# Performance work log

Hardware: AMD Instinct MI355X
Metric: run time of the kernel (lower is better)

## Reference

```python
import jax, jax.numpy as jnp
import numpy as np

K = 12          # tagset size incl START/STOP
START = 10
STOP = 11
NEG = -10000.0
B, T, V, D, H = 64, 1024, 50000, 256, 512
Hh = H // 2


def setup_inputs() -> dict:
    key = jax.random.key(0)
    ks = jax.random.split(key, 20)
    sentence = jax.random.randint(ks[0], (B, T), 1, V)
    seq_lens = jax.random.randint(ks[1], (B,), T // 2, T + 1)
    emb = jax.random.normal(ks[2], (V, D), dtype=jnp.float32) * 0.1
    emb = emb.at[0].set(0.0)  # padding_idx=0
    s = 1.0 / np.sqrt(Hh)

    def u(k, shape):
        return jax.random.uniform(k, shape, minval=-s, maxval=s, dtype=jnp.float32)

    Wih_f = u(ks[3], (4 * Hh, D)); Whh_f = u(ks[4], (4 * Hh, Hh))
    bih_f = u(ks[5], (4 * Hh,));  bhh_f = u(ks[6], (4 * Hh,))
    Wih_b = u(ks[7], (4 * Hh, D)); Whh_b = u(ks[8], (4 * Hh, Hh))
    bih_b = u(ks[9], (4 * Hh,));  bhh_b = u(ks[10], (4 * Hh,))
    sl = 1.0 / np.sqrt(H)
    Wtag = jax.random.uniform(ks[11], (K, H), minval=-sl, maxval=sl, dtype=jnp.float32)
    btag = jax.random.uniform(ks[12], (K,), minval=-sl, maxval=sl, dtype=jnp.float32)
    transitions = jax.random.normal(ks[13], (K, K), dtype=jnp.float32)
    transitions = transitions.at[START, :].set(NEG).at[:, STOP].set(NEG)
    h0 = jax.random.normal(ks[14], (2, B, Hh), dtype=jnp.float32)
    c0 = jax.random.normal(ks[15], (2, B, Hh), dtype=jnp.float32)
    return dict(sentence=sentence, seq_lens=seq_lens, emb=emb,
                Wih_f=Wih_f, Whh_f=Whh_f, bih_f=bih_f, bhh_f=bhh_f,
                Wih_b=Wih_b, Whh_b=Whh_b, bih_b=bih_b, bhh_b=bhh_b,
                Wtag=Wtag, btag=btag, transitions=transitions, h0=h0, c0=c0)


def _lstm_dir(x, mask, h0, c0, Wih, Whh, bih, bhh, reverse):
    # x: [B,T,D], mask: [B,T] bool. Masked steps keep the carried state
    # (equivalent to PyTorch packed-sequence semantics for positions < seq_len).
    def step(carry, inp):
        h, c = carry
        xt, mt = inp  # [B,D], [B,1]
        z = xt @ Wih.T + h @ Whh.T + bih + bhh  # [B,4Hh], torch gate order i,f,g,o
        i, f, g, o = jnp.split(z, 4, axis=-1)
        c2 = jax.nn.sigmoid(f) * c + jax.nn.sigmoid(i) * jnp.tanh(g)
        h2 = jax.nn.sigmoid(o) * jnp.tanh(c2)
        h = jnp.where(mt, h2, h)
        c = jnp.where(mt, c2, c)
        return (h, c), h
    xs = (x.transpose(1, 0, 2), mask.T[:, :, None])
    _, hs = jax.lax.scan(step, (h0, c0), xs, reverse=reverse)
    return hs.transpose(1, 0, 2)  # [B,T,Hh]


def reference(sentence, seq_lens, emb, Wih_f, Whh_f, bih_f, bhh_f,
              Wih_b, Whh_b, bih_b, bhh_b, Wtag, btag, transitions, h0, c0):
    Bn, Tn = sentence.shape
    mask = jnp.arange(Tn)[None, :] < seq_lens[:, None]  # [B,T]
    x = emb[sentence]  # [B,T,D]
    hf = _lstm_dir(x, mask, h0[0], c0[0], Wih_f, Whh_f, bih_f, bhh_f, False)
    hb = _lstm_dir(x, mask, h0[1], c0[1], Wih_b, Whh_b, bih_b, bhh_b, True)
    feats = jnp.concatenate([hf, hb], -1) @ Wtag.T + btag  # [B,T,K]

    # Vectorized Viterbi over batch and tags (replaces per-tag python loops)
    fv0 = jnp.full((Bn, K), NEG, dtype=feats.dtype).at[:, START].set(0.0)
    ident = jnp.arange(K)[None, :]

    def vstep(fv, inp):
        ft, mt = inp  # [B,K], [B]
        sc = fv[:, None, :] + transitions[None, :, :]  # [B,Knext,Kprev]
        bp = jnp.argmax(sc, -1)                        # [B,K]
        vmax = jnp.max(sc, -1) + ft
        fv2 = jnp.where(mt[:, None], vmax, fv)
        bp = jnp.where(mt[:, None], bp, ident)         # identity passthrough on pad
        return fv2, bp

    fv, bptrs = jax.lax.scan(vstep, fv0, (feats.transpose(1, 0, 2), mask.T))
    term = fv + transitions[STOP][None, :]
    best = jnp.argmax(term, -1)   # [B]
    score = jnp.max(term, -1)     # [B]

    def btrace(tag, bp):
        prev = jnp.take_along_axis(bp, tag[:, None], 1)[:, 0]
        return prev, tag

    _, path = jax.lax.scan(btrace, best, bptrs, reverse=True)  # [T,B]
    path = jnp.where(mask, path.T, 0)  # [B,T], zeros beyond seq_len
    return score, path
```

## Files before the change

### kernel.cpp

```cpp
#include <hip/hip_runtime.h>
#include <math.h>

#define NEG10K -10000.0f

static const size_t OFF_WT_IH = 0;
static const size_t OFF_WT_HH = 524288;
static const size_t OFF_BIAS  = 1048576;
static const size_t OFF_WTAGD = 1050624;
static const size_t OFF_BTAG  = 1058816;
static const size_t OFF_FEATS = 1058832;
static const size_t OFF_HC    = 3155984;
static const size_t OFF_CC    = 3188752;
static const size_t OFF_PUB   = 3221520;
static const size_t OFF_END   = 3352592;

__device__ __forceinline__ float sigf(float x) { return 1.0f / (1.0f + expf(-x)); }

__global__ __launch_bounds__(256) void k_transpose(
    const float* __restrict__ wih_f, const float* __restrict__ wih_b,
    const float* __restrict__ whh_f, const float* __restrict__ whh_b,
    float* __restrict__ ws) {
  __shared__ float tile[32][33];
  int z = blockIdx.z;
  const float* src = (z == 0) ? wih_f : (z == 1) ? wih_b : (z == 2) ? whh_f : whh_b;
  float* dst = ws + ((z < 2) ? (OFF_WT_IH + (size_t)z * 262144)
                             : (OFF_WT_HH + (size_t)(z - 2) * 262144));
  int r0 = blockIdx.y * 32;
  int c0 = blockIdx.x * 32;
  int tid = threadIdx.x;
  int c = tid & 31, rg = tid >> 5;
#pragma unroll
  for (int i = 0; i < 4; ++i) {
    int r = rg * 4 + i;
    tile[r][c] = src[(size_t)(r0 + r) * 256 + c0 + c];
  }
  __syncthreads();
  int r2 = tid & 31, cg = tid >> 5;
#pragma unroll
  for (int i = 0; i < 4; ++i) {
    int ccv = cg * 4 + i;
    dst[(size_t)(c0 + ccv) * 1024 + r0 + r2] = tile[r2][ccv];
  }
}

__global__ __launch_bounds__(256) void k_prep_small(
    const float* __restrict__ bih_f, const float* __restrict__ bhh_f,
    const float* __restrict__ bih_b, const float* __restrict__ bhh_b,
    const float* __restrict__ wtag, const float* __restrict__ btag,
    float* __restrict__ ws) {
  int i = blockIdx.x * 256 + threadIdx.x;
  if (i < 2048) {
    int d = i >> 10, n = i & 1023;
    ws[OFF_BIAS + i] = d ? (bih_b[n] + bhh_b[n]) : (bih_f[n] + bhh_f[n]);
  } else if (i < 2048 + 8192) {
    int r = i - 2048;
    int d = r >> 12, rem = r & 4095;
    int k = rem >> 8, j = rem & 255;
    ws[OFF_WTAGD + r] = (k < 12) ? wtag[(size_t)k * 512 + d * 256 + j] : 0.0f;
  } else if (i < 2048 + 8192 + 16) {
    int kk = i - 10240;
    ws[OFF_BTAG + kk] = (kk < 12) ? btag[kk] : 0.0f;
  } else if (i < 10256 + 131072) {
    ws[OFF_PUB + (i - 10256)] = 0.0f;
  }
}

#define FMA4(A, W, S) { A.x = fmaf(W.x, S, A.x); A.y = fmaf(W.y, S, A.y); \
                        A.z = fmaf(W.z, S, A.z); A.w = fmaf(W.w, S, A.w); }
__global__ __launch_bounds__(512, 2) void k_lstm_split(
    const float* __restrict__ ws_c, const int* __restrict__ sentence,
    const float* __restrict__ emb, const float* __restrict__ h0p,
    const float* __restrict__ c0p, const int* __restrict__ seq_lens,
    float* __restrict__ ws_mut, int first) {
  __shared__ float zpart[8][4][128];
  __shared__ float zs[4][128];
  __shared__ float h_s[4][256];
  __shared__ float x_s[2][4][256];
  __shared__ int   sent_s[4][1024];
  __shared__ float ldspad[10240];

  int bx = blockIdx.x;
  int w   = (bx >> 3) & 7;
  int gid = (bx & 7) + ((bx >> 6) << 3);
  int d   = gid >> 4;
  int bq4 = (gid & 15) * 4;
  int u0  = w * 32;
  int tid = threadIdx.x;
  if (first == 777) {
    ldspad[tid] = (float)tid; __syncthreads(); zs[0][0] = ldspad[tid ^ 1];
  }

  int cg = tid & 31, kq = tid >> 5;
  int c4 = cg * 4;
  int wv = tid >> 6, ln = tid & 63;

  for (int i = tid; i < 4096; i += 512)
    sent_s[i >> 10][i & 1023] = sentence[(size_t)(bq4 + (i >> 10)) * 1024 + (i & 1023)];
  __syncthreads();

  const float* WhhT = ws_c + OFF_WT_HH + (size_t)d * 262144;
  const float* WihT = ws_c + OFF_WT_IH + (size_t)d * 262144;
  int wcol = (cg >> 3) * 256 + u0 + (cg & 7) * 4;
  float4 wh[16], wi[16];
#pragma unroll
  for (int i = 0; i < 16; ++i) {
    wh[i] = *(const float4*)(WhhT + (size_t)(kq * 16 + i) * 1024 + wcol);
    wi[i] = *(const float4*)(WihT + (size_t)(kq * 16 + i) * 1024 + wcol);
  }

  for (int i = tid; i < 1024; i += 512) {
    int b = i >> 8, u = i & 255;
    h_s[b][u] = h0p[((size_t)d * 64 + bq4 + b) * 256 + u];
  }
  float cc = 0.0f; int mylen = 0;
  int ob = tid >> 5, ou = tid & 31;
  if (tid < 128) {
    cc = c0p[((size_t)d * 64 + bq4 + ob) * 256 + u0 + ou];
    mylen = seq_lens[bq4 + ob];
  }
  int bB = tid >> 7, jB = tid & 127;
  int colB = ((jB >> 5) << 8) + u0 + (jB & 31);
  float biasB = ws_c[OFF_BIAS + (size_t)d * 1024 + colB];
  int xb = tid >> 7, xj = (tid & 127) * 2;
  {
    int tt = d ? 1023 : 0;
    float2 v = *(const float2*)(emb + (size_t)sent_s[xb][tt] * 256 + xj);
    x_s[0][xb][xj] = v.x; x_s[0][xb][xj + 1] = v.y;
  }
  int tb_b = wv >> 1;
  int tb_k = (wv & 1) * 8 + (ln >> 3);
  int tb_j = ln & 7;
  float wtag_r[32];
  {
    const float* wtg = ws_c + OFF_WTAGD + (size_t)d * 4096 + tb_k * 256;
#pragma unroll
    for (int i = 0; i < 32; ++i) wtag_r[i] = wtg[tb_j + 8 * i];
  }
  unsigned long long* pub64 = (unsigned long long*)(ws_mut + OFF_PUB);
  float* featsD = ws_mut + OFF_FEATS + (size_t)d * 1048576;
  int gb = tid >> 8, gu = tid & 255;
  bool bail = false;
  __syncthreads();

  float4 acc_carry[4] = {{0,0,0,0},{0,0,0,0},{0,0,0,0},{0,0,0,0}};
#pragma unroll
  for (int i = 0; i < 4; ++i) {
    int k = kq * 16 + i * 4;
    float4 q0 = wi[i * 4], q1 = wi[i * 4 + 1], q2 = wi[i * 4 + 2], q3 = wi[i * 4 + 3];
#pragma unroll
    for (int b = 0; b < 4; ++b) {
      float4 xv = *(const float4*)&x_s[0][b][k];
      FMA4(acc_carry[b], q0, xv.x); FMA4(acc_carry[b], q1, xv.y);
      FMA4(acc_carry[b], q2, xv.z); FMA4(acc_carry[b], q3, xv.w);
    }
  }

  for (int s = 0; s < 1024; ++s) {
    int t = d ? (1023 - s) : s;
    int p = s & 1;
    int cur = s & 1, nxt = cur ^ 1;
    unsigned tag = (unsigned)(s + 1);
    float2 xpf;
    {
      int sn = (s + 1 < 1024) ? (s + 1) : s;
      int tn = d ? (1023 - sn) : sn;
      xpf = *(const float2*)(emb + (size_t)sent_s[xb][tn] * 256 + xj);
    }
    float4 acc[4];
#pragma unroll
    for (int b = 0; b < 4; ++b) acc[b] = acc_carry[b];
#pragma unroll
    for (int i = 0; i < 4; ++i) {
      int k = kq * 16 + i * 4;
      float4 w0 = wh[i * 4], w1 = wh[i * 4 + 1], w2 = wh[i * 4 + 2], w3 = wh[i * 4 + 3];
#pragma unroll
      for (int b = 0; b < 4; ++b) {
        float4 hv = *(const float4*)&h_s[b][k];
        FMA4(acc[b], w0, hv.x); FMA4(acc[b], w1, hv.y);
        FMA4(acc[b], w2, hv.z); FMA4(acc[b], w3, hv.w);
      }
    }
#pragma unroll
    for (int b = 0; b < 4; ++b) {
      acc[b].x += __shfl_xor(acc[b].x, 32);
      acc[b].y += __shfl_xor(acc[b].y, 32);
      acc[b].z += __shfl_xor(acc[b].z, 32);
      acc[b].w += __shfl_xor(acc[b].w, 32);
    }
    if ((tid & 32) == 0) {
#pragma unroll
      for (int b = 0; b < 4; ++b) *(float4*)&zpart[wv][b][c4] = acc[b];
    }
    __syncthreads();
    zs[bB][jB] = zpart[0][bB][jB] + zpart[1][bB][jB] + zpart[2][bB][jB] + zpart[3][bB][jB] +
                 zpart[4][bB][jB] + zpart[5][bB][jB] + zpart[6][bB][jB] + zpart[7][bB][jB] + biasB;
    x_s[nxt][xb][xj] = xpf.x; x_s[nxt][xb][xj + 1] = xpf.y;
    __syncthreads();
    if (tid < 128) {
      float zi = zs[ob][ou], zf = zs[ob][32 + ou], zg = zs[ob][64 + ou], zo = zs[ob][96 + ou];
      float cn = sigf(zf) * cc + sigf(zi) * tanhf(zg);
      float hn = sigf(zo) * tanhf(cn);
      bool m = t < mylen;
      cc = m ? cn : cc;
      float hp = m ? hn : h_s[ob][u0 + ou];
      union { float f; unsigned u; } hb; hb.f = hp;
      unsigned long long pk = ((unsigned long long)tag << 32) | (unsigned long long)hb.u;
      __hip_atomic_store(
          pub64 + (size_t)p * 32768 + ((size_t)d * 64 + bq4 + ob) * 256 + (u0 + ou),
          pk, __ATOMIC_RELAXED, __HIP_MEMORY_SCOPE_AGENT);
    }
    if (s > 0) {
      int tp = d ? (1023 - (s - 1)) : (s - 1);
      float pv = 0.0f;
#pragma unroll
      for (int i = 0; i < 32; ++i)
        pv = fmaf(h_s[tb_b][tb_j + 8 * i], wtag_r[i], pv);
      pv += __shfl_xor(pv, 1);
      pv += __shfl_xor(pv, 2);
      pv += __shfl_xor(pv, 4);
      if (w == 0 && tb_j == 0)
        featsD[(size_t)(bq4 + tb_b) * 16384 + (size_t)tp * 16 + tb_k] = pv;
    }
    __syncthreads();
    {
      size_t base = (size_t)p * 32768 + ((size_t)d * 64 + bq4) * 256;
      size_t i0 = base + (size_t)gb * 256 + gu;
      size_t i1 = i0 + 512;
      unsigned long long v0 =
          __hip_atomic_load(pub64 + i0, __ATOMIC_RELAXED, __HIP_MEMORY_SCOPE_AGENT);
      unsigned long long v1 =
          __hip_atomic_load(pub64 + i1, __ATOMIC_RELAXED, __HIP_MEMORY_SCOPE_AGENT);
      if (s + 1 < 1024) {
#pragma unroll
        for (int b = 0; b < 4; ++b) { acc_carry[b].x = 0; acc_carry[b].y = 0;
                                      acc_carry[b].z = 0; acc_carry[b].w = 0; }
#pragma unroll
        for (int i = 0; i < 4; ++i) {
          int k = kq * 16 + i * 4;
          float4 q0 = wi[i * 4], q1 = wi[i * 4 + 1], q2 = wi[i * 4 + 2], q3 = wi[i * 4 + 3];
#pragma unroll
          for (int b = 0; b < 4; ++b) {
            float4 xv = *(const float4*)&x_s[nxt][b][k];
            FMA4(acc_carry[b], q0, xv.x); FMA4(acc_carry[b], q1, xv.y);
            FMA4(acc_carry[b], q2, xv.z); FMA4(acc_carry[b], q3, xv.w);
          }
        }
      }
      unsigned spin = 0;
      while ((((unsigned)(v0 >> 32) != tag) || ((unsigned)(v1 >> 32) != tag)) && !bail) {
        __builtin_amdgcn_s_sleep(1);
        if ((unsigned)(v0 >> 32) != tag)
          v0 = __hip_atomic_load(pub64 + i0, __ATOMIC_RELAXED, __HIP_MEMORY_SCOPE_AGENT);
        if ((unsigned)(v1 >> 32) != tag)
          v1 = __hip_atomic_load(pub64 + i1, __ATOMIC_RELAXED, __HIP_MEMORY_SCOPE_AGENT);
        if (++spin > 2000000u) { bail = true; break; }
      }
      union { unsigned u32; float f; } cv0, cv1;
      cv0.u32 = (unsigned)v0; cv1.u32 = (unsigned)v1;
      h_s[gb][gu]     = cv0.f;
      h_s[gb + 2][gu] = cv1.f;
    }
    __syncthreads();
  }
  {
    float pv = 0.0f;
#pragma unroll
    for (int i = 0; i < 32; ++i)
      pv = fmaf(h_s[tb_b][tb_j + 8 * i], wtag_r[i], pv);
    pv += __shfl_xor(pv, 1);
    pv += __shfl_xor(pv, 2);
    pv += __shfl_xor(pv, 4);
    int tl = d ? 0 : 1023;
    if (w == 0 && tb_j == 0)
      featsD[(size_t)(bq4 + tb_b) * 16384 + (size_t)tl * 16 + tb_k] = pv;
  }
}

__global__ __launch_bounds__(256) void k_lstm_fused(
    const float* __restrict__ ws_c, const int* __restrict__ sentence,
    const float* __restrict__ emb, const float* __restrict__ h0p,
    const float* __restrict__ c0p, const int* __restrict__ seq_lens,
    float* __restrict__ ws_mut) {
  int d = blockIdx.x & 1;
  int pr = blockIdx.x >> 1;
  int b0 = pr * 2, b1 = b0 + 1;
  const float* Wih = ws_c + OFF_WT_IH + (size_t)d * 262144;
  const float* Whh = ws_c + OFF_WT_HH + (size_t)d * 262144;
  __shared__ float h_s[2][256];
  __shared__ float x_s[2][2][256];
  __shared__ float z_s[2][1024];
  __shared__ int   sent_s[2][1024];
  __shared__ float wt_s[16][260];
  __shared__ float pfp_s[2][16][8];
  int tid = threadIdx.x;
  int len0 = seq_lens[b0], len1 = seq_lens[b1];
  for (int i = tid; i < 2048; i += 256)
    sent_s[i >> 10][i & 1023] = sentence[(size_t)(b0 + (i >> 10)) * 1024 + (i & 1023)];
  for (int i = tid; i < 4096; i += 256)
    wt_s[i >> 8][i & 255] = ws_c[OFF_WTAGD + (size_t)d * 4096 + i];
  h_s[0][tid] = h0p[((size_t)d * 64 + b0) * 256 + tid];
  h_s[1][tid] = h0p[((size_t)d * 64 + b1) * 256 + tid];
  float cc0 = c0p[((size_t)d * 64 + b0) * 256 + tid];
  float cc1 = c0p[((size_t)d * 64 + b1) * 256 + tid];
  int c4 = tid * 4;
  float4 bias_v = *(const float4*)(ws_c + OFF_BIAS + (size_t)d * 1024 + c4);
  __syncthreads();
  int t0 = d ? 1023 : 0;
  if (tid < 128) {
    int bb = tid >> 6, l = tid & 63;
    int row = sent_s[bb][t0];
    *(float4*)&x_s[0][bb][l * 4] = *(const float4*)(emb + (size_t)row * 256 + l * 4);
  }
  __syncthreads();
  float* featsD = ws_mut + OFF_FEATS + (size_t)d * 1048576;
  for (int s = 0; s < 1024; ++s) {
    int t = d ? (1023 - s) : s;
    int cur = s & 1, nxt = cur ^ 1;
    float4 pf = {0, 0, 0, 0};
    if (tid < 128) {
      int sn = (s < 1023) ? (s + 1) : 1023;
      int tn = d ? (1023 - sn) : sn;
      int bb = tid >> 6, l = tid & 63;
      pf = *(const float4*)(emb + (size_t)sent_s[bb][tn] * 256 + l * 4);
    }
    float4 a0 = bias_v, a1 = bias_v;
#pragma unroll 4
    for (int k = 0; k < 256; k += 4) {
      float4 xv0 = *(const float4*)&x_s[cur][0][k];
      float4 xv1 = *(const float4*)&x_s[cur][1][k];
      float4 hv0 = *(const float4*)&h_s[0][k];
      float4 hv1 = *(const float4*)&h_s[1][k];
      const float* wi = Wih + (size_t)k * 1024 + c4;
      const float* wh = Whh + (size_t)k * 1024 + c4;
      float4 wi0 = *(const float4*)(wi);
      float4 wi1 = *(const float4*)(wi + 1024);
      float4 wi2 = *(const float4*)(wi + 2048);
      float4 wi3 = *(const float4*)(wi + 3072);
      float4 wh0 = *(const float4*)(wh);
      float4 wh1 = *(const float4*)(wh + 1024);
      float4 wh2 = *(const float4*)(wh + 2048);
      float4 wh3 = *(const float4*)(wh + 3072);
      FMA4(a0, wi0, xv0.x); FMA4(a0, wi1, xv0.y); FMA4(a0, wi2, xv0.z); FMA4(a0, wi3, xv0.w);
      FMA4(a0, wh0, hv0.x); FMA4(a0, wh1, hv0.y); FMA4(a0, wh2, hv0.z); FMA4(a0, wh3, hv0.w);
      FMA4(a1, wi0, xv1.x); FMA4(a1, wi1, xv1.y); FMA4(a1, wi2, xv1.z); FMA4(a1, wi3, xv1.w);
      FMA4(a1, wh0, hv1.x); FMA4(a1, wh1, hv1.y); FMA4(a1, wh2, hv1.z); FMA4(a1, wh3, hv1.w);
    }
    *(float4*)&z_s[0][c4] = a0;
    *(float4*)&z_s[1][c4] = a1;
    __syncthreads();
    {
      float iv = z_s[0][tid], fv = z_s[0][tid + 256];
      float gv = z_s[0][tid + 512], ov = z_s[0][tid + 768];
      float cn = sigf(fv) * cc0 + sigf(iv) * tanhf(gv);
      float hn = sigf(ov) * tanhf(cn);
      bool m = t < len0;
      cc0 = m ? cn : cc0;
      h_s[0][tid] = m ? hn : h_s[0][tid];
    }
    {
      float iv = z_s[1][tid], fv = z_s[1][tid + 256];
      float gv = z_s[1][tid + 512], ov = z_s[1][tid + 768];
      float cn = sigf(fv) * cc1 + sigf(iv) * tanhf(gv);
      float hn = sigf(ov) * tanhf(cn);
      bool m = t < len1;
      cc1 = m ? cn : cc1;
      h_s[1][tid] = m ? hn : h_s[1][tid];
    }
    if (tid < 128) {
      int bb = tid >> 6, l = tid & 63;
      *(float4*)&x_s[nxt][bb][l * 4] = pf;
    }
    __syncthreads();
    {
      int b2 = tid >> 7, r = tid & 127;
      int ks = r >> 3, jg = r & 7;
      const float* hv = &h_s[b2][jg * 32];
      const float* wv = &wt_s[ks][jg * 32];
      float p = 0.0f;
#pragma unroll
      for (int i = 0; i < 32; ++i) p = fmaf(hv[i], wv[i], p);
      pfp_s[b2][ks][jg] = p;
    }
    __syncthreads();
    if (tid < 32) {
      int b = tid >> 4, k = tid & 15;
      float sum = 0.0f;
#pragma unroll
      for (int i = 0; i < 8; ++i) sum += pfp_s[b][k][i];
      featsD[(size_t)(b0 + b) * 16384 + (size_t)t * 16 + k] = sum;
    }
  }
}

__global__ __launch_bounds__(64) void k_viterbi(const float* __restrict__ ws_c,
                                                const float* __restrict__ trans,
                                                const int* __restrict__ seq_lens,
                                                float* __restrict__ out) {
  __shared__ char bp_s[1024][12];
  int b = blockIdx.x, lane = threadIdx.x;
  int len = seq_lens[b];
  float trow[12];
#pragma unroll
  for (int p = 0; p < 12; ++p) trow[p] = (lane < 12) ? trans[lane * 12 + p] : 0.0f;
  float tb = (lane < 16) ? ws_c[OFF_BTAG + lane] : 0.0f;
  float fv = (lane == 10) ? 0.0f : NEG10K;
  const float* ff = ws_c + OFF_FEATS + (size_t)b * 16384;
  const float* fb = ws_c + OFF_FEATS + 1048576 + (size_t)b * 16384;
  for (int t = 0; t < 1024; ++t) {
    float ft = (lane < 16) ? (ff[t * 16 + lane] + fb[t * 16 + lane] + tb) : 0.0f;
    float best = -3.0e38f; int arg = 0;
#pragma unroll
    for (int p = 0; p < 12; ++p) {
      float s = __shfl(fv, p) + trow[p];
      if (s > best) { best = s; arg = p; }
    }
    bool m = t < len;
    if (m) fv = best + ft;
    if (lane < 12) bp_s[t][lane] = (char)(m ? arg : lane);
  }
  float term = (lane < 12) ? fv + trans[132 + lane] : -3.0e38f;
  float bestv = -3.0e38f; int bestp = 0;
#pragma unroll
  for (int p = 0; p < 12; ++p) {
    float v = __shfl(term, p);
    if (v > bestv) { bestv = v; bestp = p; }
  }
  __syncthreads();
  if (lane == 0) {
    out[b] = bestv;
    int tag = bestp;
    float* po = out + 64 + (size_t)b * 1024;
    for (int t = 1023; t >= 0; --t) {
      po[t] = (t < len) ? (float)tag : 0.0f;
      tag = bp_s[t][tag];
    }
  }
}

extern "C" void kernel_launch(void* const* d_in, const int* in_sizes, int n_in,
                              void* d_out, int out_size, void* d_ws, size_t ws_size,
                              hipStream_t stream) {
  (void)in_sizes; (void)n_in; (void)out_size;
  const int*   sentence = (const int*)d_in[0];
  const int*   seq_lens = (const int*)d_in[1];
  const float* emb      = (const float*)d_in[2];
  const float* wih_f    = (const float*)d_in[3];
  const float* whh_f    = (const float*)d_in[4];
  const float* bih_f    = (const float*)d_in[5];
  const float* bhh_f    = (const float*)d_in[6];
  const float* wih_b    = (const float*)d_in[7];
  const float* whh_b    = (const float*)d_in[8];
  const float* bih_b    = (const float*)d_in[9];
  const float* bhh_b    = (const float*)d_in[10];
  const float* wtag     = (const float*)d_in[11];
  const float* btag     = (const float*)d_in[12];
  const float* trans    = (const float*)d_in[13];
  const float* h0p      = (const float*)d_in[14];
  const float* c0p      = (const float*)d_in[15];
  float* ws  = (float*)d_ws;
  float* out = (float*)d_out;
  size_t avail = ws_size / 4;
  if (avail < OFF_FEATS + 2097152) return;

  k_transpose<<<dim3(8, 32, 4), 256, 0, stream>>>(wih_f, wih_b, whh_f, whh_b, ws);
  k_prep_small<<<553, 256, 0, stream>>>(bih_f, bhh_f, bih_b, bhh_b, wtag, btag, ws);
  if (avail >= OFF_END) {
    k_lstm_split<<<256, 512, 0, stream>>>(ws, sentence, emb, h0p, c0p, seq_lens, ws, 1);
  } else {
    k_lstm_fused<<<64, 256, 0, stream>>>(ws, sentence, emb, h0p, c0p, seq_lens, ws);
  }
  k_viterbi<<<64, 64, 0, stream>>>(ws, trans, seq_lens, out);
}
```

Baseline: 3.650 ms.

## Split LSTM recurrence across 512 blocks of 256 threads with 16 units each

Re-partitions the persistent split LSTM kernel so each block owns 16 hidden units instead of 32. The grid doubles to 512 blocks of 256 threads, halving per-block work per timestep and the per-step reduction depth. The tag projection weights move from registers into shared memory and only w==0 blocks compute feats. The cost is twice as many blocks taking part in the cross-block spin-wait exchange every step, and each thread now polls four published values instead of two.

```diff
diff --git a/kernel.cpp b/kernel.cpp
--- a/kernel.cpp
+++ b/kernel.cpp
@@ -67,40 +67,44 @@
 
 #define FMA4(A, W, S) { A.x = fmaf(W.x, S, A.x); A.y = fmaf(W.y, S, A.y); \
                         A.z = fmaf(W.z, S, A.z); A.w = fmaf(W.w, S, A.w); }
-__global__ __launch_bounds__(512, 2) void k_lstm_split(
+__global__ __launch_bounds__(256, 2) void k_lstm_split(
     const float* __restrict__ ws_c, const int* __restrict__ sentence,
     const float* __restrict__ emb, const float* __restrict__ h0p,
     const float* __restrict__ c0p, const int* __restrict__ seq_lens,
     float* __restrict__ ws_mut, int first) {
-  __shared__ float zpart[8][4][128];
-  __shared__ float zs[4][128];
+  __shared__ float zpart[4][4][64];
+  __shared__ float zs[4][64];
   __shared__ float h_s[4][256];
   __shared__ float x_s[2][4][256];
   __shared__ int   sent_s[4][1024];
-  __shared__ float ldspad[10240];
+  __shared__ float wt_s[16][260];
+  __shared__ float ldspad[6400];
 
   int bx = blockIdx.x;
-  int w   = (bx >> 3) & 7;
-  int gid = (bx & 7) + ((bx >> 6) << 3);
+  int w   = (bx >> 3) & 15;
+  int gid = (bx & 7) + ((bx >> 7) << 3);
   int d   = gid >> 4;
   int bq4 = (gid & 15) * 4;
-  int u0  = w * 32;
+  int u0  = w * 16;
   int tid = threadIdx.x;
+  int ln  = tid & 63;
   if (first == 777) {
     ldspad[tid] = (float)tid; __syncthreads(); zs[0][0] = ldspad[tid ^ 1];
   }
 
-  int cg = tid & 31, kq = tid >> 5;
+  int cg = tid & 15, kq = tid >> 4;
   int c4 = cg * 4;
-  int wv = tid >> 6, ln = tid & 63;
-
-  for (int i = tid; i < 4096; i += 512)
+  int wv = tid >> 6;
+
+  for (int i = tid; i < 4096; i += 256)
     sent_s[i >> 10][i & 1023] = sentence[(size_t)(bq4 + (i >> 10)) * 1024 + (i & 1023)];
+  for (int i = tid; i < 4096; i += 256)
+    wt_s[i >> 8][i & 255] = ws_c[OFF_WTAGD + (size_t)d * 4096 + i];
   __syncthreads();
 
   const float* WhhT = ws_c + OFF_WT_HH + (size_t)d * 262144;
   const float* WihT = ws_c + OFF_WT_IH + (size_t)d * 262144;
-  int wcol = (cg >> 3) * 256 + u0 + (cg & 7) * 4;
+  int wcol = (cg >> 2) * 256 + u0 + (cg & 3) * 4;
   float4 wh[16], wi[16];
 #pragma unroll
   for (int i = 0; i < 16; ++i) {
@@ -108,37 +112,23 @@
     wi[i] = *(const float4*)(WihT + (size_t)(kq * 16 + i) * 1024 + wcol);
   }
 
-  for (int i = tid; i < 1024; i += 512) {
-    int b = i >> 8, u = i & 255;
-    h_s[b][u] = h0p[((size_t)d * 64 + bq4 + b) * 256 + u];
-  }
+  for (int i = tid; i < 1024; i += 256)
+    h_s[i >> 8][i & 255] = h0p[((size_t)d * 64 + bq4 + (i >> 8)) * 256 + (i & 255)];
   float cc = 0.0f; int mylen = 0;
-  int ob = tid >> 5, ou = tid & 31;
-  if (tid < 128) {
+  int ob = tid >> 4, ou = tid & 15;
+  if (tid < 64) {
     cc = c0p[((size_t)d * 64 + bq4 + ob) * 256 + u0 + ou];
     mylen = seq_lens[bq4 + ob];
   }
-  int bB = tid >> 7, jB = tid & 127;
-  int colB = ((jB >> 5) << 8) + u0 + (jB & 31);
-  float biasB = ws_c[OFF_BIAS + (size_t)d * 1024 + colB];
-  int xb = tid >> 7, xj = (tid & 127) * 2;
+  int bB = tid >> 6, jB = tid & 63;
+  float biasB = ws_c[OFF_BIAS + (size_t)d * 1024 + (jB >> 4) * 256 + u0 + (jB & 15)];
+  int xb = tid >> 6, xj = (tid & 63) * 4;
   {
     int tt = d ? 1023 : 0;
-    float2 v = *(const float2*)(emb + (size_t)sent_s[xb][tt] * 256 + xj);
-    x_s[0][xb][xj] = v.x; x_s[0][xb][xj + 1] = v.y;
-  }
-  int tb_b = wv >> 1;
-  int tb_k = (wv & 1) * 8 + (ln >> 3);
-  int tb_j = ln & 7;
-  float wtag_r[32];
-  {
-    const float* wtg = ws_c + OFF_WTAGD + (size_t)d * 4096 + tb_k * 256;
-#pragma unroll
-    for (int i = 0; i < 32; ++i) wtag_r[i] = wtg[tb_j + 8 * i];
+    *(float4*)&x_s[0][xb][xj] = *(const float4*)(emb + (size_t)sent_s[xb][tt] * 256 + xj);
   }
   unsigned long long* pub64 = (unsigned long long*)(ws_mut + OFF_PUB);
   float* featsD = ws_mut + OFF_FEATS + (size_t)d * 1048576;
-  int gb = tid >> 8, gu = tid & 255;
   bool bail = false;
   __syncthreads();
 
@@ -158,13 +148,13 @@
   for (int s = 0; s < 1024; ++s) {
     int t = d ? (1023 - s) : s;
     int p = s & 1;
-    int cur = s & 1, nxt = cur ^ 1;
+    int nxt = (s & 1) ^ 1;
     unsigned tag = (unsigned)(s + 1);
-    float2 xpf;
+    float4 xpf;
     {
       int sn = (s + 1 < 1024) ? (s + 1) : s;
       int tn = d ? (1023 - sn) : sn;
-      xpf = *(const float2*)(emb + (size_t)sent_s[xb][tn] * 256 + xj);
+      xpf = *(const float4*)(emb + (size_t)sent_s[xb][tn] * 256 + xj);
     }
     float4 acc[4];
 #pragma unroll
@@ -182,22 +172,26 @@
     }
 #pragma unroll
     for (int b = 0; b < 4; ++b) {
+      acc[b].x += __shfl_xor(acc[b].x, 16);
+      acc[b].y += __shfl_xor(acc[b].y, 16);
+      acc[b].z += __shfl_xor(acc[b].z, 16);
+      acc[b].w += __shfl_xor(acc[b].w, 16);
       acc[b].x += __shfl_xor(acc[b].x, 32);
       acc[b].y += __shfl_xor(acc[b].y, 32);
       acc[b].z += __shfl_xor(acc[b].z, 32);
       acc[b].w += __shfl_xor(acc[b].w, 32);
     }
-    if ((tid & 32) == 0) {
+    if ((tid & 48) == 0) {
 #pragma unroll
       for (int b = 0; b < 4; ++b) *(float4*)&zpart[wv][b][c4] = acc[b];
     }
     __syncthreads();
     zs[bB][jB] = zpart[0][bB][jB] + zpart[1][bB][jB] + zpart[2][bB][jB] + zpart[3][bB][jB] +
-                 zpart[4][bB][jB] + zpart[5][bB][jB] + zpart[6][bB][jB] + zpart[7][bB][jB] + biasB;
-    x_s[nxt][xb][xj] = xpf.x; x_s[nxt][xb][xj + 1] = xpf.y;
-    __syncthreads();
-    if (tid < 128) {
-      float zi = zs[ob][ou], zf = zs[ob][32 + ou], zg = zs[ob][64 + ou], zo = zs[ob][96 + ou];
+                 biasB;
+    *(float4*)&x_s[nxt][xb][xj] = xpf;
+    __syncthreads();
+    if (tid < 64) {
+      float zi = zs[ob][ou], zf = zs[ob][16 + ou], zg = zs[ob][32 + ou], zo = zs[ob][48 + ou];
       float cn = sigf(zf) * cc + sigf(zi) * tanhf(zg);
       float hn = sigf(zo) * tanhf(cn);
       bool m = t < mylen;
@@ -209,27 +203,36 @@
           pub64 + (size_t)p * 32768 + ((size_t)d * 64 + bq4 + ob) * 256 + (u0 + ou),
           pk, __ATOMIC_RELAXED, __HIP_MEMORY_SCOPE_AGENT);
     }
-    if (s > 0) {
+    if (w == 0 && s > 0) {
       int tp = d ? (1023 - (s - 1)) : (s - 1);
-      float pv = 0.0f;
-#pragma unroll
-      for (int i = 0; i < 32; ++i)
-        pv = fmaf(h_s[tb_b][tb_j + 8 * i], wtag_r[i], pv);
-      pv += __shfl_xor(pv, 1);
-      pv += __shfl_xor(pv, 2);
-      pv += __shfl_xor(pv, 4);
-      if (w == 0 && tb_j == 0)
-        featsD[(size_t)(bq4 + tb_b) * 16384 + (size_t)tp * 16 + tb_k] = pv;
+#pragma unroll
+      for (int half = 0; half < 2; ++half) {
+        int vs = wv + 4 * half;
+        int tb_b = vs >> 1;
+        int tb_k = (vs & 1) * 8 + (ln >> 3);
+        int tb_j = ln & 7;
+        float pv = 0.0f;
+#pragma unroll
+        for (int i = 0; i < 32; ++i)
+          pv = fmaf(h_s[tb_b][tb_j + 8 * i], wt_s[tb_k][tb_j + 8 * i], pv);
+        pv += __shfl_xor(pv, 1);
+        pv += __shfl_xor(pv, 2);
+        pv += __shfl_xor(pv, 4);
+        if (tb_j == 0)
+          featsD[(size_t)(bq4 + tb_b) * 16384 + (size_t)tp * 16 + tb_k] = pv;
+      }
     }
     __syncthreads();
     {
-      size_t base = (size_t)p * 32768 + ((size_t)d * 64 + bq4) * 256;
-      size_t i0 = base + (size_t)gb * 256 + gu;
-      size_t i1 = i0 + 512;
+      size_t base = (size_t)p * 32768 + ((size_t)d * 64 + bq4) * 256 + tid;
       unsigned long long v0 =
-          __hip_atomic_load(pub64 + i0, __ATOMIC_RELAXED, __HIP_MEMORY_SCOPE_AGENT);
+          __hip_atomic_load(pub64 + base,       __ATOMIC_RELAXED, __HIP_MEMORY_SCOPE_AGENT);
       unsigned long long v1 =
-          __hip_atomic_load(pub64 + i1, __ATOMIC_RELAXED, __HIP_MEMORY_SCOPE_AGENT);
+          __hip_atomic_load(pub64 + base + 256, __ATOMIC_RELAXED, __HIP_MEMORY_SCOPE_AGENT);
+      unsigned long long v2 =
+          __hip_atomic_load(pub64 + base + 512, __ATOMIC_RELAXED, __HIP_MEMORY_SCOPE_AGENT);
+      unsigned long long v3 =
+          __hip_atomic_load(pub64 + base + 768, __ATOMIC_RELAXED, __HIP_MEMORY_SCOPE_AGENT);
       if (s + 1 < 1024) {
 #pragma unroll
         for (int b = 0; b < 4; ++b) { acc_carry[b].x = 0; acc_carry[b].y = 0;
@@ -247,32 +250,45 @@
         }
       }
       unsigned spin = 0;
-      while ((((unsigned)(v0 >> 32) != tag) || ((unsigned)(v1 >> 32) != tag)) && !bail) {
+      while ((((unsigned)(v0 >> 32) != tag) || ((unsigned)(v1 >> 32) != tag) ||
+              ((unsigned)(v2 >> 32) != tag) || ((unsigned)(v3 >> 32) != tag)) && !bail) {
         __builtin_amdgcn_s_sleep(1);
         if ((unsigned)(v0 >> 32) != tag)
-          v0 = __hip_atomic_load(pub64 + i0, __ATOMIC_RELAXED, __HIP_MEMORY_SCOPE_AGENT);
+          v0 = __hip_atomic_load(pub64 + base,       __ATOMIC_RELAXED, __HIP_MEMORY_SCOPE_AGENT);
         if ((unsigned)(v1 >> 32) != tag)
-          v1 = __hip_atomic_load(pub64 + i1, __ATOMIC_RELAXED, __HIP_MEMORY_SCOPE_AGENT);
+          v1 = __hip_atomic_load(pub64 + base + 256, __ATOMIC_RELAXED, __HIP_MEMORY_SCOPE_AGENT);
+        if ((unsigned)(v2 >> 32) != tag)
+          v2 = __hip_atomic_load(pub64 + base + 512, __ATOMIC_RELAXED, __HIP_MEMORY_SCOPE_AGENT);
+        if ((unsigned)(v3 >> 32) != tag)
+          v3 = __hip_atomic_load(pub64 + base + 768, __ATOMIC_RELAXED, __HIP_MEMORY_SCOPE_AGENT);
         if (++spin > 2000000u) { bail = true; break; }
       }
-      union { unsigned u32; float f; } cv0, cv1;
-      cv0.u32 = (unsigned)v0; cv1.u32 = (unsigned)v1;
-      h_s[gb][gu]     = cv0.f;
-      h_s[gb + 2][gu] = cv1.f;
-    }
-    __syncthreads();
-  }
-  {
-    float pv = 0.0f;
-#pragma unroll
-    for (int i = 0; i < 32; ++i)
-      pv = fmaf(h_s[tb_b][tb_j + 8 * i], wtag_r[i], pv);
-    pv += __shfl_xor(pv, 1);
-    pv += __shfl_xor(pv, 2);
-    pv += __shfl_xor(pv, 4);
+      union { unsigned u32; float f; } cv;
+      cv.u32 = (unsigned)v0; h_s[0][tid] = cv.f;
+      cv.u32 = (unsigned)v1; h_s[1][tid] = cv.f;
+      cv.u32 = (unsigned)v2; h_s[2][tid] = cv.f;
+      cv.u32 = (unsigned)v3; h_s[3][tid] = cv.f;
+    }
+    __syncthreads();
+  }
+  if (w == 0) {
     int tl = d ? 0 : 1023;
-    if (w == 0 && tb_j == 0)
-      featsD[(size_t)(bq4 + tb_b) * 16384 + (size_t)tl * 16 + tb_k] = pv;
+#pragma unroll
+    for (int half = 0; half < 2; ++half) {
+      int vs = wv + 4 * half;
+      int tb_b = vs >> 1;
+      int tb_k = (vs & 1) * 8 + (ln >> 3);
+      int tb_j = ln & 7;
+      float pv = 0.0f;
+#pragma unroll
+      for (int i = 0; i < 32; ++i)
+        pv = fmaf(h_s[tb_b][tb_j + 8 * i], wt_s[tb_k][tb_j + 8 * i], pv);
+      pv += __shfl_xor(pv, 1);
+      pv += __shfl_xor(pv, 2);
+      pv += __shfl_xor(pv, 4);
+      if (tb_j == 0)
+        featsD[(size_t)(bq4 + tb_b) * 16384 + (size_t)tl * 16 + tb_k] = pv;
+    }
   }
 }
 
@@ -465,7 +481,7 @@
   k_transpose<<<dim3(8, 32, 4), 256, 0, stream>>>(wih_f, wih_b, whh_f, whh_b, ws);
   k_prep_small<<<553, 256, 0, stream>>>(bih_f, bhh_f, bih_b, bhh_b, wtag, btag, ws);
   if (avail >= OFF_END) {
-    k_lstm_split<<<256, 512, 0, stream>>>(ws, sentence, emb, h0p, c0p, seq_lens, ws, 1);
+    k_lstm_split<<<512, 256, 0, stream>>>(ws, sentence, emb, h0p, c0p, seq_lens, ws, 1);
   } else {
     k_lstm_fused<<<64, 256, 0, stream>>>(ws, sentence, emb, h0p, c0p, seq_lens, ws);
   }
```

Result: slower. 4.995 ms (+36.9%).
